# Optimization experiments

Hardware: AMD Instinct MI355X
Metric: run time of the kernel (lower is better)

## Reference

```python
import jax, jax.numpy as jnp
import numpy as np

GROUP = 4      # number of groups in the batch dim
SHARED_GP = 4  # conv groups for q/k 1x1 convs
C = 512
N = 4096
B = 4          # B_all = GROUP * B = 16
EPS_LN = 1e-6
EPS_Z = 1e-6


def _phi(x):
    return jax.nn.relu(x) + 1.0


def _grouped_1x1(x, W):
    # x: [B, C, N], W: [g, C/g, C/g] block-diagonal 1x1 conv weights
    Bx, Cx, Nx = x.shape
    g = W.shape[0]
    xg = x.reshape(Bx, g, Cx // g, Nx)
    return jnp.einsum('goc,bgcn->bgon', W, xg).reshape(Bx, Cx, Nx)


def _ln(x, w, b, eps=EPS_LN):
    m = jnp.mean(x, axis=-1, keepdims=True)
    v = jnp.mean(jnp.square(x - m), axis=-1, keepdims=True)
    return (x - m) * jax.lax.rsqrt(v + eps) * w + b


def setup_inputs() -> dict:
    key = jax.random.key(0)
    ks = jax.random.split(key, 12)
    cg = C // SHARED_GP
    s = 1.0 / np.sqrt(C)
    return {
        'x': jax.random.normal(ks[0], (GROUP * B, C, N), dtype=jnp.float32),
        'Wq': jax.random.normal(ks[1], (SHARED_GP, cg, cg), dtype=jnp.float32) / np.sqrt(cg),
        'Wk': jax.random.normal(ks[2], (SHARED_GP, cg, cg), dtype=jnp.float32) / np.sqrt(cg),
        'Wv': jax.random.normal(ks[3], (C, C), dtype=jnp.float32) * s,
        'Wphi': jax.random.normal(ks[4], (C, C), dtype=jnp.float32) * s,
        'ln1_w': jnp.ones((C,), dtype=jnp.float32),
        'ln1_b': jnp.zeros((C,), dtype=jnp.float32),
        'fc1_w': jax.random.normal(ks[5], (4 * C, C), dtype=jnp.float32) * s,
        'fc1_b': jnp.zeros((4 * C,), dtype=jnp.float32),
        'fc2_w': jax.random.normal(ks[6], (C, 4 * C), dtype=jnp.float32) / np.sqrt(4 * C),
        'fc2_b': jnp.zeros((C,), dtype=jnp.float32),
        'ln2_w': jnp.ones((C,), dtype=jnp.float32),
        'ln2_b': jnp.zeros((C,), dtype=jnp.float32),
    }


def reference(x, Wq, Wk, Wv, Wphi, ln1_w, ln1_b, fc1_w, fc1_b, fc2_w, fc2_b, ln2_w, ln2_b):
    B_all, Cc, Nn = x.shape
    g = GROUP
    Bb = B_all // g
    first, rest = x[:Bb], x[Bb:]             # [B,C,N], [M,C,N] with M=(g-1)*B
    M = (g - 1) * Bb

    q = _phi(_grouped_1x1(rest, Wq))          # [M,C,N]
    k0 = _phi(_grouped_1x1(first, Wk))        # [B,C,N]
    v0 = jnp.einsum('oc,bcn->bon', Wv, first)  # [B,C,N]
    phi_first = jnp.einsum('oc,bcn->bon', Wphi, first)
    phi_rest = jnp.einsum('oc,bcn->bon', Wphi, rest)

    # expand first-group k/v across the (g-1) query groups
    k = jnp.broadcast_to(k0[None], (g - 1, Bb, Cc, Nn)).reshape(M, Cc, Nn)
    v = jnp.broadcast_to(v0[None], (g - 1, Bb, Cc, Nn)).reshape(M, Cc, Nn)

    Qg = jnp.broadcast_to(k0.mean(axis=2, keepdims=True)[None],
                          (g - 1, Bb, Cc, 1)).reshape(M, Cc, 1)
    alpha = jax.nn.softmax(jnp.sum(Qg * k, axis=1, keepdims=True), axis=-1) * Nn  # [M,1,N]
    k_hat = k * alpha

    # linear attention: kv = k_hat @ v^T / sqrt(C)
    kv = jnp.einsum('mcn,mdn->mcd', k_hat, v) / jnp.sqrt(jnp.asarray(Cc, x.dtype))  # [M,C,C]
    k_sum = jnp.sum(k_hat, axis=-1)                                  # [M,C]
    z = 1.0 / (jnp.einsum('mcn,mc->mn', q, k_sum)[:, None, :] + EPS_Z)  # [M,1,N]
    y = jnp.einsum('mcn,mcd->mdn', q, kv) * z * phi_rest              # [M,C,N]

    y_first = jnp.mean(y, axis=0, keepdims=True) * phi_first          # [B,C,N]
    out_first = _ln((first + y_first).transpose(0, 2, 1), ln1_w, ln1_b)  # [B,N,C]
    h = jax.nn.relu(out_first @ fc1_w.T + fc1_b)
    out_first = out_first + h @ fc2_w.T + fc2_b
    out_first = jax.nn.relu(_ln(out_first, ln2_w, ln2_b))
    out_first = out_first.transpose(0, 2, 1)                          # [B,C,N]
    return jnp.concatenate([out_first, rest], axis=0)
```

## Files before the change

kernel.cpp:

```cpp
#include <hip/hip_runtime.h>

#define N_DIM 4096
#define C_DIM 512
#define CN_ ((long)C_DIM * (long)N_DIM)

typedef unsigned short ushort_t;
typedef __attribute__((ext_vector_type(8))) short bf16x8;
typedef __attribute__((ext_vector_type(4))) float f32x4;

typedef const __attribute__((address_space(1))) unsigned int* gas_t;
typedef __attribute__((address_space(3))) unsigned int* las_t;
#define GLOAD(g, l) __builtin_amdgcn_global_load_lds((gas_t)(g), (las_t)(l), 16, 0, 0)

__device__ __forceinline__ ushort_t f2b(float f) {
    unsigned u = __builtin_bit_cast(unsigned, f);
    u += 0x7fffu + ((u >> 16) & 1u);
    return (ushort_t)(u >> 16);
}
__device__ __forceinline__ float b2f(ushort_t s) {
    return __builtin_bit_cast(float, (unsigned)s << 16);
}

enum { EPI_NONE = 0, EPI_PHI = 1, EPI_RELU_BIAS = 2, EPI_RES_BIAS = 3, EPI_PRE = 4 };

#define SBAR { __builtin_amdgcn_sched_barrier(0); __builtin_amdgcn_s_barrier(); __builtin_amdgcn_sched_barrier(0); }
#define WAITV0 { asm volatile("s_waitcnt vmcnt(0)" ::: "memory"); __builtin_amdgcn_sched_barrier(0); }
#define WAITV4 { asm volatile("s_waitcnt vmcnt(4)" ::: "memory"); __builtin_amdgcn_sched_barrier(0); }
#define WAITV8 { asm volatile("s_waitcnt vmcnt(8)" ::: "memory"); __builtin_amdgcn_sched_barrier(0); }

#define STAGE(q, koff) { \
    GLOAD(ap0 + (koff), &Als[q][la0]); \
    GLOAD(ap1 + (koff), &Als[q][la1]); \
    GLOAD(bp0 + (koff), &Bls[q][la0]); \
    GLOAD(bp1 + (koff), &Bls[q][la1]); }

#define COMPUTE(q) { \
    bf16x8 af[4], bfv[4]; \
    _Pragma("unroll") for (int m_ = 0; m_ < 4; ++m_) \
        af[m_] = *(const bf16x8*)&Als[q][(wr + m_ * 16 + fr) * 32 + rsw]; \
    _Pragma("unroll") for (int nf_ = 0; nf_ < 4; ++nf_) \
        bfv[nf_] = *(const bf16x8*)&Bls[q][(wc + nf_ * 16 + fr) * 32 + rsw]; \
    _Pragma("unroll") for (int m_ = 0; m_ < 4; ++m_) \
        _Pragma("unroll") for (int nf_ = 0; nf_ < 4; ++nf_) \
            acc[m_][nf_] = __builtin_amdgcn_mfma_f32_16x16x32_bf16( \
                af[m_], bfv[nf_], acc[m_][nf_], 0, 0, 0); }

#define KLOOP(K_) { \
    const int S_ = (K_) / 32; \
    STAGE(0, 0); \
    if (S_ > 1) STAGE(1, 32); \
    int s_ = 0; \
    while (true) { \
        if (s_ + 1 < S_) { WAITV4 } else { WAITV0 } \
        SBAR; \
        COMPUTE(s_ & 1); \
        SBAR; \
        if (s_ + 2 < S_) STAGE(s_ & 1, (s_ + 2) * 32); \
        ++s_; \
        if (s_ >= S_) break; \
    } }

template<int EPI, bool GROUPED, bool OBF, bool DEN, bool QGS>
__global__ __launch_bounds__(256, 3) void mfma_gemm(
    const ushort_t* __restrict__ Wb, const ushort_t* __restrict__ A,
    void* __restrict__ OUTV, const float* __restrict__ bias,
    const ushort_t* __restrict__ auxb, const float* __restrict__ auxf,
    int K, int O, int a_rstride, long a_zstride, long o_zstride, long auxb_zstride,
    int xt, int yt)
{
    __shared__ ushort_t Als[2][128 * 32];
    __shared__ ushort_t Bls[2][128 * 32];
    const int tid = threadIdx.x;

    const int L = blockIdx.x;
    const int gpx = (gridDim.x >> 3) / xt;
    const int xcd = L & 7;
    const int j = L >> 3;
    const int xtile = j % xt;
    const int g = xcd * gpx + j / xt;
    const int ytile = g % yt;
    const int z = g / yt;

    const int o0 = xtile * 128;
    const int n0 = ytile * 128;
    const ushort_t* Az = A + (long)z * a_zstride;
    const ushort_t* Wp = Wb;
    int kbase = 0, obase = o0;
    if (GROUPED) { int gg = o0 >> 7; Wp = Wb + (long)gg * (128 * 128); kbase = gg << 7; obase = 0; }

    const int w = tid >> 6, l = tid & 63;
    const int lr = l >> 2, lg = l & 3;
    const int rA0 = w * 32 + lr, rA1 = w * 32 + 16 + lr;
    const int gA0 = lg ^ ((rA0 >> 1) & 3), gA1 = lg ^ ((rA1 >> 1) & 3);
    const ushort_t* ap0 = Az + (long)(n0 + rA0) * a_rstride + kbase + gA0 * 8;
    const ushort_t* ap1 = Az + (long)(n0 + rA1) * a_rstride + kbase + gA1 * 8;
    const ushort_t* bp0 = Wp + (long)(obase + rA0) * K + gA0 * 8;
    const ushort_t* bp1 = Wp + (long)(obase + rA1) * K + gA1 * 8;
    const int la0 = (w * 32) * 32, la1 = (w * 32 + 16) * 32;

    const int wr = (w >> 1) * 64, wc = (w & 1) * 64;
    const int fr = l & 15, ks = l >> 4;
    const int rsw = (ks ^ ((fr >> 1) & 3)) << 3;

    f32x4 acc[4][4];
#pragma unroll
    for (int m = 0; m < 4; ++m)
#pragma unroll
        for (int nf = 0; nf < 4; ++nf) acc[m][nf] = f32x4{0.f, 0.f, 0.f, 0.f};

    KLOOP(K);

    float dsum[4][4];
    if (DEN) {
#pragma unroll
        for (int m = 0; m < 4; ++m)
#pragma unroll
            for (int j2 = 0; j2 < 4; ++j2) dsum[m][j2] = 0.f;
    }
    float qsum[4];
    if (QGS) {
#pragma unroll
        for (int nf = 0; nf < 4; ++nf) qsum[nf] = 0.f;
    }

#pragma unroll
    for (int m = 0; m < 4; ++m) {
#pragma unroll
        for (int nf = 0; nf < 4; ++nf) {
            const int oo = o0 + wc + nf * 16 + fr;
            float bval = 0.f;
            if (EPI == EPI_RELU_BIAS || EPI == EPI_RES_BIAS) bval = bias[oo];
            float kw = 0.f;
            if (DEN) kw = bias[((z & 3) << 9) + oo];
#pragma unroll
            for (int j2 = 0; j2 < 4; ++j2) {
                const int nn = n0 + wr + m * 16 + ks * 4 + j2;
                const long ridx = (long)nn * O + oo;
                float v = acc[m][nf][j2];
                if (EPI == EPI_PHI)            v = fmaxf(v, 0.f) + 1.f;
                else if (EPI == EPI_RELU_BIAS) v = fmaxf(v + bval, 0.f);
                else if (EPI == EPI_RES_BIAS)  v = v + bval + b2f(auxb[(long)z * auxb_zstride + ridx]);
                else if (EPI == EPI_PRE)       v = b2f(auxb[(long)z * auxb_zstride + ridx]) + auxf[ridx] * v;
                if (DEN) dsum[m][j2] += v * kw;
                if (QGS) qsum[nf] += v;
                if (OBF) ((ushort_t*)OUTV)[(long)z * o_zstride + ridx] = f2b(v);
                else     ((float*)OUTV)[(long)z * o_zstride + ridx] = v;
            }
        }
    }

    if (DEN) {
#pragma unroll
        for (int m = 0; m < 4; ++m)
#pragma unroll
            for (int j2 = 0; j2 < 4; ++j2) {
                float d = dsum[m][j2];
                d += __shfl_xor(d, 1); d += __shfl_xor(d, 2);
                d += __shfl_xor(d, 4); d += __shfl_xor(d, 8);
                if (fr == 0) {
                    const int nn = n0 + wr + m * 16 + ks * 4 + j2;
                    atomicAdd((float*)&auxf[(long)z * N_DIM + nn], d);
                }
            }
    }
    if (QGS) {
#pragma unroll
        for (int nf = 0; nf < 4; ++nf) {
            float d = qsum[nf];
            d += __shfl_xor(d, 16);
            d += __shfl_xor(d, 32);
            if (ks == 0) {
                const int oo = o0 + wc + nf * 16 + fr;
                atomicAdd((float*)&auxf[((long)z << 9) + oo], d);
            }
        }
    }
}

__global__ __launch_bounds__(256, 3) void kv_mfma(
    const ushort_t* __restrict__ v0c, const ushort_t* __restrict__ khat,
    float* __restrict__ kvp)
{
    __shared__ ushort_t Als[2][128 * 32];
    __shared__ ushort_t Bls[2][128 * 32];
    const int tid = threadIdx.x;
    const int L = blockIdx.x;
    const int gpx = (gridDim.x >> 3) >> 2;
    const int xcd = L & 7;
    const int j = L >> 3;
    const int xtile = j & 3;
    const int g = xcd * gpx + (j >> 2);
    const int ytile = g & 3;
    const int z = g >> 2;
    const int c0 = xtile * 128, d0 = ytile * 128;
    const int b = z >> 3, nch = z & 7;

    const int w = tid >> 6, l = tid & 63;
    const int lr = l >> 2, lg = l & 3;
    const int rA0 = w * 32 + lr, rA1 = w * 32 + 16 + lr;
    const int gA0 = lg ^ ((rA0 >> 1) & 3), gA1 = lg ^ ((rA1 >> 1) & 3);
    const ushort_t* Ab = v0c + (long)b * CN_ + nch * 512;
    const ushort_t* Bb = khat + (long)b * CN_ + nch * 512;
    const ushort_t* ap0 = Ab + (long)(d0 + rA0) * N_DIM + gA0 * 8;
    const ushort_t* ap1 = Ab + (long)(d0 + rA1) * N_DIM + gA1 * 8;
    const ushort_t* bp0 = Bb + (long)(c0 + rA0) * N_DIM + gA0 * 8;
    const ushort_t* bp1 = Bb + (long)(c0 + rA1) * N_DIM + gA1 * 8;
    const int la0 = (w * 32) * 32, la1 = (w * 32 + 16) * 32;

    const int wr = (w >> 1) * 64, wc = (w & 1) * 64;
    const int fr = l & 15, ks = l >> 4;
    const int rsw = (ks ^ ((fr >> 1) & 3)) << 3;

    f32x4 acc[4][4];
#pragma unroll
    for (int m = 0; m < 4; ++m)
#pragma unroll
        for (int nf = 0; nf < 4; ++nf) acc[m][nf] = f32x4{0.f, 0.f, 0.f, 0.f};

    KLOOP(512);

    float* KV = kvp + ((long)(nch * 4 + b)) * 262144;
#pragma unroll
    for (int m = 0; m < 4; ++m)
#pragma unroll
        for (int nf = 0; nf < 4; ++nf) {
            const int cc = c0 + wc + nf * 16 + fr;
#pragma unroll
            for (int j2 = 0; j2 < 4; ++j2) {
                const int dd = d0 + wr + m * 16 + ks * 4 + j2;
                KV[(long)dd * 512 + cc] = acc[m][nf][j2];
            }
        }
}

__global__ __launch_bounds__(256) void cvt_scale8(
    const float* __restrict__ kvp, ushort_t* __restrict__ out)
{
    const float s = 0.044194173824159216f;
    const long i = ((long)blockIdx.x * 256 + threadIdx.x) * 4;
    const int b = (int)(i >> 18);
    const long j = i & 262143;
    float4 a = make_float4(0.f, 0.f, 0.f, 0.f);
#pragma unroll
    for (int nch = 0; nch < 8; ++nch) {
        float4 v = *(const float4*)&kvp[((long)(nch * 4 + b)) * 262144 + j];
        a.x += v.x; a.y += v.y; a.z += v.z; a.w += v.w;
    }
    union { ushort_t sh[4]; uint2 u; } p;
    p.sh[0] = f2b(a.x * s); p.sh[1] = f2b(a.y * s);
    p.sh[2] = f2b(a.z * s); p.sh[3] = f2b(a.w * s);
    *(uint2*)&out[i] = p.u;
}

__global__ __launch_bounds__(256, 2) void ybar_gemm(
    const ushort_t* __restrict__ q12, const ushort_t* __restrict__ kvT,
    const ushort_t* __restrict__ xT12, const ushort_t* __restrict__ Wphi_b,
    const float* __restrict__ den12, ushort_t* __restrict__ y12)
{
    __shared__ ushort_t Als[2][128 * 32];
    __shared__ ushort_t Bls[2][128 * 32];
    __shared__ ushort_t Cls[2][128 * 32];
    __shared__ ushort_t Dls[2][128 * 32];
    const int tid = threadIdx.x;
    const int L = blockIdx.x;
    const int gpx = (gridDim.x >> 3) >> 2;
    const int xcd = L & 7;
    const int j = L >> 3;
    const int xtile = j & 3;
    const int g = xcd * gpx + (j >> 2);
    const int ytile = g & 31;
    const int mm = g >> 5;
    const int o0 = xtile * 128, n0 = ytile * 128;

    const int w = tid >> 6, l = tid & 63;
    const int lr = l >> 2, lg = l & 3;
    const int rA0 = w * 32 + lr, rA1 = w * 32 + 16 + lr;
    const int gA0 = lg ^ ((rA0 >> 1) & 3), gA1 = lg ^ ((rA1 >> 1) & 3);
    const long aoff0 = (long)(n0 + rA0) * 512 + gA0 * 8;
    const long aoff1 = (long)(n0 + rA1) * 512 + gA1 * 8;
    const long boff0 = (long)(o0 + rA0) * 512 + gA0 * 8;
    const long boff1 = (long)(o0 + rA1) * 512 + gA1 * 8;
    const int la0 = (w * 32) * 32, la1 = (w * 32 + 16) * 32;

    const int wr = (w >> 1) * 64, wc = (w & 1) * 64;
    const int fr = l & 15, ks = l >> 4;
    const int rsw = (ks ^ ((fr >> 1) & 3)) << 3;

    const ushort_t* pa0 = xT12 + (long)mm * CN_ + aoff0;
    const ushort_t* pa1 = xT12 + (long)mm * CN_ + aoff1;
    const ushort_t* pb0 = Wphi_b + boff0;
    const ushort_t* pb1 = Wphi_b + boff1;
    const ushort_t* qa0 = q12 + (long)mm * CN_ + aoff0;
    const ushort_t* qa1 = q12 + (long)mm * CN_ + aoff1;
    const ushort_t* kb0 = kvT + (long)(mm & 3) * 262144 + boff0;
    const ushort_t* kb1 = kvT + (long)(mm & 3) * 262144 + boff1;

    f32x4 accP[4][4], accQ[4][4];
#pragma unroll
    for (int m = 0; m < 4; ++m)
#pragma unroll
        for (int nf = 0; nf < 4; ++nf) {
            accP[m][nf] = f32x4{0.f, 0.f, 0.f, 0.f};
            accQ[m][nf] = f32x4{0.f, 0.f, 0.f, 0.f};
        }

#define STAGE2(q, koff) { \
    GLOAD(pa0 + (koff), &Als[q][la0]); GLOAD(pa1 + (koff), &Als[q][la1]); \
    GLOAD(pb0 + (koff), &Bls[q][la0]); GLOAD(pb1 + (koff), &Bls[q][la1]); \
    GLOAD(qa0 + (koff), &Cls[q][la0]); GLOAD(qa1 + (koff), &Cls[q][la1]); \
    GLOAD(kb0 + (koff), &Dls[q][la0]); GLOAD(kb1 + (koff), &Dls[q][la1]); }

#define COMPUTE2(q) { \
    bf16x8 af[4], bfv[4], cf[4], df[4]; \
    _Pragma("unroll") for (int m_ = 0; m_ < 4; ++m_) { \
        af[m_] = *(const bf16x8*)&Als[q][(wr + m_ * 16 + fr) * 32 + rsw]; \
        cf[m_] = *(const bf16x8*)&Cls[q][(wr + m_ * 16 + fr) * 32 + rsw]; } \
    _Pragma("unroll") for (int nf_ = 0; nf_ < 4; ++nf_) { \
        bfv[nf_] = *(const bf16x8*)&Bls[q][(wc + nf_ * 16 + fr) * 32 + rsw]; \
        df[nf_] = *(const bf16x8*)&Dls[q][(wc + nf_ * 16 + fr) * 32 + rsw]; } \
    _Pragma("unroll") for (int m_ = 0; m_ < 4; ++m_) \
        _Pragma("unroll") for (int nf_ = 0; nf_ < 4; ++nf_) { \
            accP[m_][nf_] = __builtin_amdgcn_mfma_f32_16x16x32_bf16( \
                af[m_], bfv[nf_], accP[m_][nf_], 0, 0, 0); \
            accQ[m_][nf_] = __builtin_amdgcn_mfma_f32_16x16x32_bf16( \
                cf[m_], df[nf_], accQ[m_][nf_], 0, 0, 0); } }

    STAGE2(0, 0);
    STAGE2(1, 32);
    int s_ = 0;
    while (true) {
        if (s_ + 1 < 16) { WAITV8 } else { WAITV0 }
        SBAR;
        COMPUTE2(s_ & 1);
        SBAR;
        if (s_ + 2 < 16) STAGE2(s_ & 1, (s_ + 2) * 32);
        ++s_;
        if (s_ >= 16) break;
    }
#undef STAGE2
#undef COMPUTE2

    const float* D = den12 + (long)mm * N_DIM;
    ushort_t* Y = y12 + (long)mm * CN_;
#pragma unroll
    for (int m = 0; m < 4; ++m) {
        float zr[4];
#pragma unroll
        for (int j2 = 0; j2 < 4; ++j2)
            zr[j2] = 1.f / (D[n0 + wr + m * 16 + ks * 4 + j2] + 1e-6f);
#pragma unroll
        for (int nf = 0; nf < 4; ++nf) {
            const int oo = o0 + wc + nf * 16 + fr;
#pragma unroll
            for (int j2 = 0; j2 < 4; ++j2) {
                const int nn = n0 + wr + m * 16 + ks * 4 + j2;
                Y[(long)nn * 512 + oo] = f2b(accQ[m][nf][j2] * zr[j2] * accP[m][nf][j2]);
            }
        }
    }
}

__global__ __launch_bounds__(256) void ybar_reduce(
    const ushort_t* __restrict__ y12, float* __restrict__ ybar)
{
    const long i = ((long)blockIdx.x * 256 + threadIdx.x) * 8;
    float s[8] = {0.f, 0.f, 0.f, 0.f, 0.f, 0.f, 0.f, 0.f};
    for (int mm = 0; mm < 12; ++mm) {
        uint4 u = *(const uint4*)&y12[(long)mm * CN_ + i];
        const ushort_t* us = (const ushort_t*)&u;
#pragma unroll
        for (int j = 0; j < 8; ++j) s[j] += b2f(us[j]);
    }
#pragma unroll
    for (int j = 0; j < 8; ++j) s[j] *= (1.f / 12.f);
    *(float4*)&ybar[i] = make_float4(s[0], s[1], s[2], s[3]);
    *(float4*)&ybar[i + 4] = make_float4(s[4], s[5], s[6], s[7]);
}

template<int ALPHA>
__global__ __launch_bounds__(256) void transpose_b2b(
    const ushort_t* __restrict__ in, ushort_t* __restrict__ out,
    const float* __restrict__ alpha, float* __restrict__ ksum)
{
    __shared__ ushort_t t[64][72];
    const int tid = threadIdx.x;
    const int n0 = blockIdx.x * 64, c0 = blockIdx.y * 64, z = blockIdx.z;
    const ushort_t* I = in + (long)z * CN_;
    ushort_t* O = out + (long)z * CN_;
    const int r = tid >> 2, s8 = (tid & 3) * 16;
    uint4 u0 = *(const uint4*)&I[(long)(n0 + r) * 512 + c0 + s8];
    uint4 u1 = *(const uint4*)&I[(long)(n0 + r) * 512 + c0 + s8 + 8];
    *(uint4*)&t[r][s8] = u0;
    *(uint4*)&t[r][s8 + 8] = u1;
    __syncthreads();
    union { ushort_t sh[16]; uint4 u[2]; } p;
#pragma unroll
    for (int i = 0; i < 16; ++i) {
        ushort_t v = t[s8 + i][r];
        if (ALPHA) v = f2b(b2f(v) * alpha[(long)z * N_DIM + n0 + s8 + i]);
        p.sh[i] = v;
    }
    uint4* dst = (uint4*)&O[(long)(c0 + r) * N_DIM + n0 + s8];
    dst[0] = p.u[0]; dst[1] = p.u[1];
    if (ALPHA) {
        const int c = tid & 63, q = tid >> 6;
        float s = 0.f;
#pragma unroll
        for (int i = 0; i < 16; ++i) {
            const int n = q * 16 + i;
            s += b2f(t[n][c]) * alpha[(long)z * N_DIM + n0 + n];
        }
        atomicAdd(&ksum[((long)z << 9) + c0 + c], s);
    }
}

__global__ __launch_bounds__(256) void cvt_all(
    const float* __restrict__ s0, ushort_t* __restrict__ d0,
    const float* __restrict__ s1, ushort_t* __restrict__ d1,
    const float* __restrict__ s2, ushort_t* __restrict__ d2,
    const float* __restrict__ s3, ushort_t* __restrict__ d3,
    const float* __restrict__ s4, ushort_t* __restrict__ d4,
    const float* __restrict__ s5, ushort_t* __restrict__ d5)
{
    long i = ((long)blockIdx.x * 256 + threadIdx.x) * 4;
    const float* s; ushort_t* d; long off;
    if (i < 65536)        { s = s0; d = d0; off = i; }
    else if (i < 131072)  { s = s1; d = d1; off = i - 65536; }
    else if (i < 393216)  { s = s2; d = d2; off = i - 131072; }
    else if (i < 655360)  { s = s3; d = d3; off = i - 393216; }
    else if (i < 1703936) { s = s4; d = d4; off = i - 655360; }
    else                  { s = s5; d = d5; off = i - 1703936; }
    float4 v = *(const float4*)&s[off];
    union { ushort_t sh[4]; uint2 u; } p;
    p.sh[0] = f2b(v.x); p.sh[1] = f2b(v.y); p.sh[2] = f2b(v.z); p.sh[3] = f2b(v.w);
    *(uint2*)&d[off] = p.u;
}

template<int PASSZ>
__global__ __launch_bounds__(256) void transpose_f2b(
    const float* __restrict__ in, ushort_t* __restrict__ out,
    int rows, int cols, long in_z, long out_z, float* __restrict__ passout)
{
    __shared__ float t[64][65];
    const int tid = threadIdx.x;
    const int n0 = blockIdx.x * 64, c0 = blockIdx.y * 64;
    const int z = blockIdx.z;
    const float* I = in + (long)z * in_z;
    ushort_t* Ot = out + (long)z * out_z;
    const int r = tid >> 2, s4 = (tid & 3) * 16;
    float4 raw[4];
#pragma unroll
    for (int i = 0; i < 16; i += 4) {
        float4 v = *(const float4*)&I[(long)(c0 + r) * cols + n0 + s4 + i];
        raw[i >> 2] = v;
        t[r][s4 + i] = v.x; t[r][s4 + i + 1] = v.y;
        t[r][s4 + i + 2] = v.z; t[r][s4 + i + 3] = v.w;
    }
    if (PASSZ && z >= 4) {
        float* P = passout + (long)z * in_z + (long)(c0 + r) * cols + n0 + s4;
#pragma unroll
        for (int i = 0; i < 4; ++i) *(float4*)&P[i * 4] = raw[i];
    }
    __syncthreads();
    union { ushort_t s[16]; uint4 u[2]; } pk;
#pragma unroll
    for (int i = 0; i < 16; ++i) pk.s[i] = f2b(t[s4 + i][r]);
    uint4* dst = (uint4*)&Ot[(long)(n0 + r) * rows + c0 + s4];
    dst[0] = pk.u[0]; dst[1] = pk.u[1];
}

__global__ __launch_bounds__(256) void dot_rows(
    const ushort_t* __restrict__ X, const float* __restrict__ w,
    float* __restrict__ out, float scale)
{
    const int tid = threadIdx.x;
    const int rn = tid >> 2, cs = (tid & 3) * 128;
    const int z = blockIdx.y;
    const int n = blockIdx.x * 64 + rn;
    const ushort_t* row = X + (long)z * CN_ + (long)n * C_DIM;
    const float* wz = w + (long)(z & 3) * C_DIM;
    float s = 0.f;
    for (int i = 0; i < 128; i += 8) {
        uint4 u = *(const uint4*)&row[cs + i];
        const ushort_t* us = (const ushort_t*)&u;
#pragma unroll
        for (int k2 = 0; k2 < 8; ++k2) s += b2f(us[k2]) * wz[cs + i + k2];
    }
    s += __shfl_xor(s, 1); s += __shfl_xor(s, 2);
    if ((tid & 3) == 0) out[(long)z * N_DIM + n] = s * scale;
}

__global__ __launch_bounds__(256) void softmax_alpha(
    const float* __restrict__ logits, float* __restrict__ alpha)
{
    int b = blockIdx.x, tid = threadIdx.x;
    const float* L = logits + (long)b * N_DIM;
    float* A = alpha + (long)b * N_DIM;
    float lv[16];
    float mx = -3.4e38f;
#pragma unroll
    for (int i = 0; i < 4; i++) {
        float4 v = *(const float4*)&L[tid * 4 + i * 1024];
        lv[4 * i + 0] = v.x; lv[4 * i + 1] = v.y; lv[4 * i + 2] = v.z; lv[4 * i + 3] = v.w;
        mx = fmaxf(mx, fmaxf(fmaxf(v.x, v.y), fmaxf(v.z, v.w)));
    }
    __shared__ float red[8];
    float m = mx;
#pragma unroll
    for (int off = 32; off; off >>= 1) m = fmaxf(m, __shfl_down(m, off, 64));
    int wid = tid >> 6, lane = tid & 63;
    if (lane == 0) red[wid] = m;
    __syncthreads();
    m = fmaxf(fmaxf(red[0], red[1]), fmaxf(red[2], red[3]));
    float e[16], s = 0.f;
#pragma unroll
    for (int i = 0; i < 16; i++) { e[i] = expf(lv[i] - m); s += e[i]; }
#pragma unroll
    for (int off = 32; off; off >>= 1) s += __shfl_down(s, off, 64);
    if (lane == 0) red[4 + wid] = s;
    __syncthreads();
    float S = red[4] + red[5] + red[6] + red[7];
    float sc = 4096.f / S;
#pragma unroll
    for (int i = 0; i < 4; i++)
        *(float4*)&A[tid * 4 + i * 1024] =
            make_float4(e[4 * i] * sc, e[4 * i + 1] * sc, e[4 * i + 2] * sc, e[4 * i + 3] * sc);
}

template<int RELU, int OBF, int IBF>
__global__ __launch_bounds__(256) void ln_row(
    const void* __restrict__ inv, const float* __restrict__ g,
    const float* __restrict__ bt, void* __restrict__ outv)
{
    const int tid = threadIdx.x;
    const int r = tid >> 3, cs = (tid & 7) * 64;
    const long base = (((long)blockIdx.y * N_DIM) + blockIdx.x * 32 + r) * C_DIM + cs;
    float vv[64];
    float s = 0.f, s2 = 0.f;
    if (IBF) {
        const ushort_t* I = (const ushort_t*)inv + base;
#pragma unroll
        for (int i = 0; i < 8; ++i) {
            uint4 u = *(const uint4*)&I[i * 8];
            const ushort_t* us = (const ushort_t*)&u;
#pragma unroll
            for (int jj = 0; jj < 8; ++jj) {
                float f = b2f(us[jj]); vv[i * 8 + jj] = f; s += f; s2 += f * f;
            }
        }
    } else {
        const float* I = (const float*)inv + base;
#pragma unroll
        for (int i = 0; i < 16; ++i) {
            float4 v = *(const float4*)&I[i * 4];
            vv[i * 4] = v.x; vv[i * 4 + 1] = v.y; vv[i * 4 + 2] = v.z; vv[i * 4 + 3] = v.w;
            s += v.x + v.y + v.z + v.w;
            s2 += v.x * v.x + v.y * v.y + v.z * v.z + v.w * v.w;
        }
    }
#pragma unroll
    for (int off = 1; off < 8; off <<= 1) { s += __shfl_xor(s, off); s2 += __shfl_xor(s2, off); }
    const float mean = s * (1.f / 512.f);
    const float var = s2 * (1.f / 512.f) - mean * mean;
    const float rs = rsqrtf(var + 1e-6f);
#pragma unroll
    for (int i = 0; i < 64; i += 4) {
        float o[4];
#pragma unroll
        for (int jj = 0; jj < 4; ++jj) {
            float ov = (vv[i + jj] - mean) * rs * g[cs + i + jj] + bt[cs + i + jj];
            if (RELU) ov = fmaxf(ov, 0.f);
            o[jj] = ov;
        }
        if (OBF) {
            union { ushort_t s4[4]; uint2 u; } p;
            p.s4[0] = f2b(o[0]); p.s4[1] = f2b(o[1]); p.s4[2] = f2b(o[2]); p.s4[3] = f2b(o[3]);
            *(uint2*)&((ushort_t*)outv)[base + i] = p.u;
        } else {
            *(float4*)&((float*)outv)[base + i] = make_float4(o[0], o[1], o[2], o[3]);
        }
    }
}

__global__ __launch_bounds__(256) void ln_tr(
    const ushort_t* __restrict__ in, const float* __restrict__ g,
    const float* __restrict__ bt, float* __restrict__ out)
{
    __shared__ float t[32][513];
    const int tid = threadIdx.x;
    const int r = tid >> 3;
    const int lc = (tid & 7) * 8;
    const int z = blockIdx.y;
    const long n = (long)blockIdx.x * 32 + r;
    const ushort_t* I = in + ((long)z * N_DIM + n) * C_DIM;
    float vv[64];
    float s = 0.f, s2 = 0.f;
#pragma unroll
    for (int i = 0; i < 8; ++i) {
        const int c = i * 64 + lc;
        uint4 u = *(const uint4*)&I[c];
        const ushort_t* us = (const ushort_t*)&u;
#pragma unroll
        for (int jj = 0; jj < 8; ++jj) {
            float f = b2f(us[jj]); vv[i * 8 + jj] = f; s += f; s2 += f * f;
        }
    }
#pragma unroll
    for (int off = 1; off < 8; off <<= 1) { s += __shfl_xor(s, off); s2 += __shfl_xor(s2, off); }
    const float mean = s * (1.f / 512.f);
    const float var = s2 * (1.f / 512.f) - mean * mean;
    const float rs = rsqrtf(var + 1e-6f);
#pragma unroll
    for (int i = 0; i < 8; ++i) {
        const int c = i * 64 + lc;
#pragma unroll
        for (int jj = 0; jj < 8; ++jj) {
            float o = (vv[i * 8 + jj] - mean) * rs * g[c + jj] + bt[c + jj];
            t[r][c + jj] = fmaxf(o, 0.f);
        }
    }
    __syncthreads();
    float* O = out + (long)z * CN_ + (long)blockIdx.x * 32;
    for (int c = tid; c < 512; c += 256) {
        float* dst = O + (long)c * N_DIM;
#pragma unroll
        for (int i = 0; i < 32; i += 4)
            *(float4*)&dst[i] = make_float4(t[i][c], t[i + 1][c], t[i + 2][c], t[i + 3][c]);
    }
}

extern "C" void kernel_launch(void* const* d_in, const int* in_sizes, int n_in,
                              void* d_out, int out_size, void* d_ws, size_t ws_size,
                              hipStream_t stream)
{
    const float* x     = (const float*)d_in[0];
    const float* Wq    = (const float*)d_in[1];
    const float* Wk    = (const float*)d_in[2];
    const float* Wv    = (const float*)d_in[3];
    const float* Wphi  = (const float*)d_in[4];
    const float* ln1_w = (const float*)d_in[5];
    const float* ln1_b = (const float*)d_in[6];
    const float* fc1_w = (const float*)d_in[7];
    const float* fc1_bias = (const float*)d_in[8];
    const float* fc2_w = (const float*)d_in[9];
    const float* fc2_bias = (const float*)d_in[10];
    const float* ln2_w = (const float*)d_in[11];
    const float* ln2_b = (const float*)d_in[12];
    float* out = (float*)d_out;

    float* ws = (float*)d_ws;
    const long CN = CN_;
    ushort_t* xTfirst = (ushort_t*)ws;
    ushort_t* tln     = (ushort_t*)ws;
    ushort_t* xT12 = (ushort_t*)(ws + 2 * CN);
    ushort_t* hbuf4 = (ushort_t*)(ws + 2 * CN);
    ushort_t* q12   = (ushort_t*)(ws + 8 * CN);
    ushort_t* y12   = (ushort_t*)(ws + 14 * CN);
    ushort_t* k0b = (ushort_t*)(ws + 20 * CN);
    ushort_t* v0b = (ushort_t*)(ws + 22 * CN);
    ushort_t* pre_b = (ushort_t*)(ws + 20 * CN);
    ushort_t* khat = (ushort_t*)(ws + 24 * CN);
    ushort_t* v0c  = (ushort_t*)(ws + 26 * CN);
    ushort_t* ubuf_b = (ushort_t*)(ws + 24 * CN);
    float* ybar = ws + 32 * CN;
    float* kvp  = ws + 33 * CN;
    ushort_t* kvT = (ushort_t*)(ws + 33 * CN + 8388608);
    float* wb = ws + 33 * CN + 8388608 + 524288;
    ushort_t* Wk_b   = (ushort_t*)(wb);
    ushort_t* Wq_b   = (ushort_t*)(wb + 32768);
    ushort_t* Wv_b   = (ushort_t*)(wb + 65536);
    ushort_t* Wphi_b = (ushort_t*)(wb + 196608);
    ushort_t* fc1_b16 = (ushort_t*)(wb + 327680);
    ushort_t* fc2_b16 = (ushort_t*)(wb + 851968);
    float* Qg     = wb + 1376256;
    float* ksum   = wb + 1378304;
    float* logits = wb + 1380352;
    float* alpha  = wb + 1396736;
    float* den12  = wb + 1413120;

    dim3 blk(256);

    cvt_all<<<2688, blk, 0, stream>>>(Wk, Wk_b, Wq, Wq_b, Wv, Wv_b,
                                      Wphi, Wphi_b, fc1_w, fc1_b16, fc2_w, fc2_b16);
    hipMemsetAsync(Qg, 0, 4096 * sizeof(float), stream);
    hipMemsetAsync(den12, 0, 49152 * sizeof(float), stream);

    transpose_f2b<1><<<dim3(64, 8, 16), blk, 0, stream>>>(
        x, xTfirst, 512, 4096, CN, CN, out);

    mfma_gemm<EPI_PHI, true, true, false, true><<<512, blk, 0, stream>>>(
        Wk_b, xTfirst, k0b, nullptr, nullptr, Qg, 128, 512, 512, CN, CN, 0, 4, 32);
    mfma_gemm<EPI_NONE, false, true, false, false><<<512, blk, 0, stream>>>(
        Wv_b, xTfirst, v0b, nullptr, nullptr, nullptr, 512, 512, 512, CN, CN, 0, 4, 32);
    dot_rows<<<dim3(64, 4), blk, 0, stream>>>(k0b, Qg, logits, 1.f / 4096.f);
    softmax_alpha<<<4, blk, 0, stream>>>(logits, alpha);
    transpose_b2b<1><<<dim3(64, 8, 4), blk, 0, stream>>>(k0b, khat, alpha, ksum);
    transpose_b2b<0><<<dim3(64, 8, 4), blk, 0, stream>>>(v0b, v0c, nullptr, nullptr);
    kv_mfma<<<512, blk, 0, stream>>>(v0c, khat, kvp);
    cvt_scale8<<<1024, blk, 0, stream>>>(kvp, kvT);

    mfma_gemm<EPI_PHI, true, true, true, false><<<1536, blk, 0, stream>>>(
        Wq_b, xT12, q12, ksum, nullptr, den12, 128, 512, 512, CN, CN, 0, 4, 32);
    ybar_gemm<<<1536, blk, 0, stream>>>(q12, kvT, xT12, Wphi_b, den12, y12);
    ybar_reduce<<<1024, blk, 0, stream>>>(y12, ybar);

    mfma_gemm<EPI_PRE, false, true, false, false><<<512, blk, 0, stream>>>(
        Wphi_b, xTfirst, pre_b, nullptr, xTfirst, ybar, 512, 512, 512, CN, CN, CN, 4, 32);
    ln_row<0, 1, 1><<<dim3(128, 4), blk, 0, stream>>>(pre_b, ln1_w, ln1_b, tln);
    mfma_gemm<EPI_RELU_BIAS, false, true, false, false><<<2048, blk, 0, stream>>>(
        fc1_b16, tln, hbuf4, fc1_bias, nullptr, nullptr,
        512, 2048, 512, CN, 8388608, 0, 16, 32);
    mfma_gemm<EPI_RES_BIAS, false, true, false, false><<<512, blk, 0, stream>>>(
        fc2_b16, hbuf4, ubuf_b, fc2_bias, tln, nullptr,
        2048, 512, 2048, 8388608, CN, CN, 4, 32);
    ln_tr<<<dim3(128, 4), blk, 0, stream>>>(ubuf_b, ln2_w, ln2_b, out);
}
```

Baseline: 452.7 us.

## Raise MFMA wave priority and retile input transpose to 128x128 bf16 LDS

Wraps the MFMA inner loops of the GEMM kernels in s_setprio(1)/s_setprio(0) so waves issuing matrix ops get scheduling priority over waves issuing loads. Separately, the fp32-to-bf16 input transpose is rewritten to use 128x128 tiles. It converts to bf16 before writing LDS, with a padded row stride, and writes the passthrough output straight from registers. The transpose aims to cut LDS footprint per element and raise work per block. The column-wise LDS reads of 16-bit values may hit bank conflicts.

```diff
diff --git a/kernel.cpp b/kernel.cpp
--- a/kernel.cpp
+++ b/kernel.cpp
@@ -40,10 +40,12 @@
         af[m_] = *(const bf16x8*)&Als[q][(wr + m_ * 16 + fr) * 32 + rsw]; \
     _Pragma("unroll") for (int nf_ = 0; nf_ < 4; ++nf_) \
         bfv[nf_] = *(const bf16x8*)&Bls[q][(wc + nf_ * 16 + fr) * 32 + rsw]; \
+    __builtin_amdgcn_s_setprio(1); \
     _Pragma("unroll") for (int m_ = 0; m_ < 4; ++m_) \
         _Pragma("unroll") for (int nf_ = 0; nf_ < 4; ++nf_) \
             acc[m_][nf_] = __builtin_amdgcn_mfma_f32_16x16x32_bf16( \
-                af[m_], bfv[nf_], acc[m_][nf_], 0, 0, 0); }
+                af[m_], bfv[nf_], acc[m_][nf_], 0, 0, 0); \
+    __builtin_amdgcn_s_setprio(0); }
 
 #define KLOOP(K_) { \
     const int S_ = (K_) / 32; \
@@ -318,12 +320,14 @@
     _Pragma("unroll") for (int nf_ = 0; nf_ < 4; ++nf_) { \
         bfv[nf_] = *(const bf16x8*)&Bls[q][(wc + nf_ * 16 + fr) * 32 + rsw]; \
         df[nf_] = *(const bf16x8*)&Dls[q][(wc + nf_ * 16 + fr) * 32 + rsw]; } \
+    __builtin_amdgcn_s_setprio(1); \
     _Pragma("unroll") for (int m_ = 0; m_ < 4; ++m_) \
         _Pragma("unroll") for (int nf_ = 0; nf_ < 4; ++nf_) { \
             accP[m_][nf_] = __builtin_amdgcn_mfma_f32_16x16x32_bf16( \
                 af[m_], bfv[nf_], accP[m_][nf_], 0, 0, 0); \
             accQ[m_][nf_] = __builtin_amdgcn_mfma_f32_16x16x32_bf16( \
-                cf[m_], df[nf_], accQ[m_][nf_], 0, 0, 0); } }
+                cf[m_], df[nf_], accQ[m_][nf_], 0, 0, 0); } \
+    __builtin_amdgcn_s_setprio(0); }
 
     STAGE2(0, 0);
     STAGE2(1, 32);
@@ -439,34 +443,34 @@
 template<int PASSZ>
 __global__ __launch_bounds__(256) void transpose_f2b(
     const float* __restrict__ in, ushort_t* __restrict__ out,
-    int rows, int cols, long in_z, long out_z, float* __restrict__ passout)
-{
-    __shared__ float t[64][65];
+    float* __restrict__ passout)
+{
+    __shared__ ushort_t t[128 * 132];
     const int tid = threadIdx.x;
-    const int n0 = blockIdx.x * 64, c0 = blockIdx.y * 64;
+    const int n0 = blockIdx.x * 128, c0 = blockIdx.y * 128;
     const int z = blockIdx.z;
-    const float* I = in + (long)z * in_z;
-    ushort_t* Ot = out + (long)z * out_z;
-    const int r = tid >> 2, s4 = (tid & 3) * 16;
-    float4 raw[4];
-#pragma unroll
-    for (int i = 0; i < 16; i += 4) {
-        float4 v = *(const float4*)&I[(long)(c0 + r) * cols + n0 + s4 + i];
-        raw[i >> 2] = v;
-        t[r][s4 + i] = v.x; t[r][s4 + i + 1] = v.y;
-        t[r][s4 + i + 2] = v.z; t[r][s4 + i + 3] = v.w;
-    }
-    if (PASSZ && z >= 4) {
-        float* P = passout + (long)z * in_z + (long)(c0 + r) * cols + n0 + s4;
-#pragma unroll
-        for (int i = 0; i < 4; ++i) *(float4*)&P[i * 4] = raw[i];
+    const int r = tid >> 1, h = (tid & 1) * 64;
+    const float* src = in + (long)z * CN_ + (long)(c0 + r) * N_DIM + n0 + h;
+    float* P = passout + (long)z * CN_ + (long)(c0 + r) * N_DIM + n0 + h;
+    const bool dopass = PASSZ && (z >= 4);
+#pragma unroll
+    for (int i = 0; i < 16; ++i) {
+        float4 v = *(const float4*)&src[i * 4];
+        if (dopass) *(float4*)&P[i * 4] = v;
+        union { ushort_t sh[4]; uint2 u; } pk;
+        pk.sh[0] = f2b(v.x); pk.sh[1] = f2b(v.y);
+        pk.sh[2] = f2b(v.z); pk.sh[3] = f2b(v.w);
+        *(uint2*)&t[r * 132 + h + i * 4] = pk.u;
     }
     __syncthreads();
-    union { ushort_t s[16]; uint4 u[2]; } pk;
-#pragma unroll
-    for (int i = 0; i < 16; ++i) pk.s[i] = f2b(t[s4 + i][r]);
-    uint4* dst = (uint4*)&Ot[(long)(n0 + r) * rows + c0 + s4];
-    dst[0] = pk.u[0]; dst[1] = pk.u[1];
+    ushort_t* dst = out + (long)z * CN_ + (long)(n0 + r) * C_DIM + c0 + h;
+#pragma unroll
+    for (int i = 0; i < 8; ++i) {
+        union { ushort_t sh[8]; uint4 u; } pk;
+#pragma unroll
+        for (int jj = 0; jj < 8; ++jj) pk.sh[jj] = t[(h + i * 8 + jj) * 132 + r];
+        *(uint4*)&dst[i * 8] = pk.u;
+    }
 }
 
 __global__ __launch_bounds__(256) void dot_rows(
@@ -685,8 +689,7 @@
     hipMemsetAsync(Qg, 0, 4096 * sizeof(float), stream);
     hipMemsetAsync(den12, 0, 49152 * sizeof(float), stream);
 
-    transpose_f2b<1><<<dim3(64, 8, 16), blk, 0, stream>>>(
-        x, xTfirst, 512, 4096, CN, CN, out);
+    transpose_f2b<1><<<dim3(32, 4, 16), blk, 0, stream>>>(x, xTfirst, out);
 
     mfma_gemm<EPI_PHI, true, true, false, true><<<512, blk, 0, stream>>>(
         Wk_b, xTfirst, k0b, nullptr, nullptr, Qg, 128, 512, 512, CN, CN, 0, 4, 32);
```

New measurement: 581.6 us. 1.28x slower.
